# Kernel optimization log

Measured on AMD Instinct MI355X. Metric: run time of the kernel, lower is better.

The kernel has to match this reference:

```python
import jax, jax.numpy as jnp
import numpy as np

B, Q, K, D, H = 16, 128, 128, 512, 512
NEG = -1e6


def setup_inputs() -> dict:
    key = jax.random.key(0)
    ks = jax.random.split(key, 7)
    return {
        "queries": jax.random.normal(ks[0], (B, Q, D), dtype=jnp.float32),
        "keys": jax.random.normal(ks[1], (B, K, D), dtype=jnp.float32),
        "values": jax.random.normal(ks[2], (B, K, D), dtype=jnp.float32),
        "valid_lens": jax.random.randint(ks[3], (B,), 1, K + 1, dtype=jnp.int32),
        "Wq": jax.random.normal(ks[4], (D, H), dtype=jnp.float32) / np.sqrt(D),
        "Wk": jax.random.normal(ks[5], (D, H), dtype=jnp.float32) / np.sqrt(D),
        "wv": jax.random.normal(ks[6], (H,), dtype=jnp.float32) / np.sqrt(H),
    }


def reference(queries, keys, values, valid_lens, Wq, Wk, wv):
    # projections (LazyLinear, bias=False)
    q = jnp.einsum("bqd,dh->bqh", queries, Wq)  # [B,Q,H]
    k = jnp.einsum("bkd,dh->bkh", keys, Wk)    # [B,K,H]
    # broadcast add -> tanh -> reduce to scalar score (Bahdanau)
    feats = jnp.tanh(q[:, :, None, :] + k[:, None, :, :])  # [B,Q,K,H]
    scores = jnp.einsum("bqkh,h->bqk", feats, wv)           # [B,Q,K]
    # masked softmax over key dim using per-batch valid lengths
    mask = jnp.arange(scores.shape[-1])[None, None, :] < valid_lens[:, None, None]
    scores = jnp.where(mask, scores, NEG)
    attn = jax.nn.softmax(scores, axis=-1)                  # [B,Q,K]
    # dropout is identity in eval mode
    return jnp.einsum("bqk,bkv->bqv", attn, values)
```

## Files before the change

### kernel.cpp

```cpp
#include <hip/hip_runtime.h>

#define Bn 16
#define Qn 128
#define Kn 128
#define Dn 512
#define Hn 512
#define NEGV (-3.0e38f)
#define PSCALE 2.8853900817779268f

typedef short s16x8 __attribute__((ext_vector_type(8)));
typedef float f32x4 __attribute__((ext_vector_type(4)));

__device__ __forceinline__ float exp2_hw(float x) {
  float r;
  asm("v_exp_f32 %0, %1" : "=v"(r) : "v"(x));
  return r;
}
__device__ __forceinline__ float rcp_hw(float x) { return __builtin_amdgcn_rcpf(x); }
__device__ __forceinline__ unsigned short f2bf(float f) {
  unsigned int u = __float_as_uint(f);
  u += 0x7fff + ((u >> 16) & 1);
  return (unsigned short)(u >> 16);
}

__global__ __launch_bounds__(256) void convert_kernel(
    const float* __restrict__ queries, const float* __restrict__ keys,
    const float* __restrict__ Wq, const float* __restrict__ Wk,
    const float* __restrict__ values,
    unsigned short* __restrict__ Abf, unsigned short* __restrict__ Wt,
    unsigned short* __restrict__ Vt)
{
  const int bid = blockIdx.x, t = threadIdx.x;
  if (bid < 512) {
    const int gid = bid * 256 + t;
    const size_t base = (size_t)gid * 16;
    const float* src = (base < 1048576) ? (queries + base) : (keys + (base - 1048576));
    unsigned short o[16];
    #pragma unroll
    for (int j = 0; j < 4; ++j) {
      float4 v = *(const float4*)(src + j * 4);
      o[j * 4 + 0] = f2bf(v.x); o[j * 4 + 1] = f2bf(v.y);
      o[j * 4 + 2] = f2bf(v.z); o[j * 4 + 3] = f2bf(v.w);
    }
    #pragma unroll
    for (int j = 0; j < 4; ++j)
      *(ushort4*)(Abf + base + j * 4) = *(ushort4*)&o[j * 4];
  } else if (bid < 640) {
    const int tid = (bid - 512) * 256 + t;
    const int n = tid & 511, rest = tid >> 9;
    const int sel = rest >> 5, k16 = rest & 31;
    const float* W = sel ? Wk : Wq;
    unsigned short o[16];
    #pragma unroll
    for (int i = 0; i < 16; ++i)
      o[i] = f2bf(W[(size_t)(k16 * 16 + i) * Hn + n]);
    unsigned short* dst = Wt + (size_t)sel * 262144 + (size_t)n * 512 + k16 * 16;
    #pragma unroll
    for (int j = 0; j < 4; ++j) *(ushort4*)(dst + j * 4) = *(ushort4*)&o[j * 4];
  } else {
    const int tid = (bid - 640) * 256 + t;
    const int d = tid & 511, rest = tid >> 9;
    const int b = rest >> 2, k32 = rest & 3;
    unsigned short o[32];
    #pragma unroll
    for (int i = 0; i < 32; ++i)
      o[i] = f2bf(values[((size_t)(b * Kn + k32 * 32 + i)) * Dn + d]);
    unsigned short* dst = Vt + (size_t)b * 65536 + (size_t)d * 128 + k32 * 32;
    #pragma unroll
    for (int j = 0; j < 8; ++j) *(ushort4*)(dst + j * 4) = *(ushort4*)&o[j * 4];
  }
}

__global__ __launch_bounds__(256) void proj_mfma(
    const unsigned short* __restrict__ Abf, const unsigned short* __restrict__ Wt,
    const float* __restrict__ wv,
    float* __restrict__ QW, float* __restrict__ Ekq)
{
  __shared__ unsigned short Al[128][72];
  __shared__ unsigned short Bl[64][72];
  __shared__ float Tep[64][132];
  const int t = threadIdx.x, w = t >> 6, l = t & 63;
  const int wm = w >> 1, wn = w & 1;
  const int rowTile = blockIdx.x;
  const int n0 = blockIdx.y * 64;
  const int R0 = rowTile * 128;
  const bool isQ = rowTile < 16;
  const unsigned short* Wsel = Wt + (isQ ? 0 : 262144);

  f32x4 acc[4][2];
  #pragma unroll
  for (int m = 0; m < 4; ++m)
    #pragma unroll
    for (int n = 0; n < 2; ++n) acc[m][n] = (f32x4)0.f;

  const int lr = l & 15, lk = l >> 4;

  for (int k0 = 0; k0 < Hn; k0 += 64) {
    ushort4 ar[4][2], br[2][2];
    #pragma unroll
    for (int i = 0; i < 4; ++i) {
      int g = t + 256 * i, r = g >> 3, c = g & 7;
      const unsigned short* p = Abf + (size_t)(R0 + r) * Hn + k0 + c * 8;
      ar[i][0] = *(const ushort4*)p; ar[i][1] = *(const ushort4*)(p + 4);
    }
    #pragma unroll
    for (int i = 0; i < 2; ++i) {
      int g = t + 256 * i, r = g >> 3, c = g & 7;
      const unsigned short* p = Wsel + (size_t)(n0 + r) * Hn + k0 + c * 8;
      br[i][0] = *(const ushort4*)p; br[i][1] = *(const ushort4*)(p + 4);
    }
    __syncthreads();
    #pragma unroll
    for (int i = 0; i < 4; ++i) {
      int g = t + 256 * i, r = g >> 3, c = g & 7;
      *(ushort4*)&Al[r][c * 8] = ar[i][0]; *(ushort4*)&Al[r][c * 8 + 4] = ar[i][1];
    }
    #pragma unroll
    for (int i = 0; i < 2; ++i) {
      int g = t + 256 * i, r = g >> 3, c = g & 7;
      *(ushort4*)&Bl[r][c * 8] = br[i][0]; *(ushort4*)&Bl[r][c * 8 + 4] = br[i][1];
    }
    __syncthreads();
    #pragma unroll
    for (int ks = 0; ks < 2; ++ks) {
      s16x8 af[4], bf_[2];
      #pragma unroll
      for (int m = 0; m < 4; ++m)
        af[m] = *(const s16x8*)&Al[wm * 64 + m * 16 + lr][ks * 32 + lk * 8];
      #pragma unroll
      for (int n = 0; n < 2; ++n)
        bf_[n] = *(const s16x8*)&Bl[wn * 32 + n * 16 + lr][ks * 32 + lk * 8];
      #pragma unroll
      for (int m = 0; m < 4; ++m)
        #pragma unroll
        for (int n = 0; n < 2; ++n)
          acc[m][n] = __builtin_amdgcn_mfma_f32_16x16x32_bf16(af[m], bf_[n], acc[m][n], 0, 0, 0);
    }
    __syncthreads();
  }

  if (isQ) {
    #pragma unroll
    for (int m = 0; m < 4; ++m)
      #pragma unroll
      for (int n = 0; n < 2; ++n)
        #pragma unroll
        for (int r = 0; r < 4; ++r) {
          int row = R0 + wm * 64 + m * 16 + lk * 4 + r;
          int col = n0 + wn * 32 + n * 16 + lr;
          float a = acc[m][n][r];
          float F  = exp2_hw(-PSCALE * a);
          float WF = -2.f * wv[col] * F;
          float2 o = {WF, F};
          *(float2*)(QW + ((size_t)row * Hn + col) * 2) = o;
        }
  } else {
    const int bb = rowTile - 16;
    #pragma unroll
    for (int m = 0; m < 4; ++m)
      #pragma unroll
      for (int n = 0; n < 2; ++n)
        #pragma unroll
        for (int r = 0; r < 4; ++r) {
          int row_l = wm * 64 + m * 16 + lk * 4 + r;
          int col_l = wn * 32 + n * 16 + lr;
          Tep[col_l][row_l] = exp2_hw(PSCALE * acc[m][n][r]);
        }
    __syncthreads();
    const int hl = t >> 2, kq = (t & 3) * 32;
    float* dst = Ekq + (size_t)bb * 65536 + (size_t)(n0 + hl) * 128 + kq;
    #pragma unroll
    for (int j = 0; j < 8; ++j)
      *(float4*)(dst + j * 4) = *(const float4*)&Tep[hl][kq + j * 4];
  }
}

struct ScoreSet { float4 e0a, e0b, e1a, e1b, qv; };

__device__ __forceinline__ void load_set(ScoreSet& s, const float* ek,
                                         const float* qwp, int hb) {
  const float* ep = ek + (size_t)(2 * hb) * 128;
  s.e0a = *(const float4*)(ep);
  s.e0b = *(const float4*)(ep + 4);
  s.e1a = *(const float4*)(ep + 128);
  s.e1b = *(const float4*)(ep + 132);
  s.qv  = *(const float4*)(qwp + 4 * hb);
}

__device__ __forceinline__ void compute_set(const ScoreSet& s, float acc[8]) {
  const float WF0 = s.qv.x, F0 = s.qv.y, WF1 = s.qv.z, F1 = s.qv.w;
  float d0, d1, num;
  d0 = F0 + s.e0a.x; d1 = F1 + s.e1a.x;
  num = __builtin_fmaf(WF0, d1, WF1 * d0);
  acc[0] = __builtin_fmaf(num, rcp_hw(d0 * d1), acc[0]);
  d0 = F0 + s.e0a.y; d1 = F1 + s.e1a.y;
  num = __builtin_fmaf(WF0, d1, WF1 * d0);
  acc[1] = __builtin_fmaf(num, rcp_hw(d0 * d1), acc[1]);
  d0 = F0 + s.e0a.z; d1 = F1 + s.e1a.z;
  num = __builtin_fmaf(WF0, d1, WF1 * d0);
  acc[2] = __builtin_fmaf(num, rcp_hw(d0 * d1), acc[2]);
  d0 = F0 + s.e0a.w; d1 = F1 + s.e1a.w;
  num = __builtin_fmaf(WF0, d1, WF1 * d0);
  acc[3] = __builtin_fmaf(num, rcp_hw(d0 * d1), acc[3]);
  d0 = F0 + s.e0b.x; d1 = F1 + s.e1b.x;
  num = __builtin_fmaf(WF0, d1, WF1 * d0);
  acc[4] = __builtin_fmaf(num, rcp_hw(d0 * d1), acc[4]);
  d0 = F0 + s.e0b.y; d1 = F1 + s.e1b.y;
  num = __builtin_fmaf(WF0, d1, WF1 * d0);
  acc[5] = __builtin_fmaf(num, rcp_hw(d0 * d1), acc[5]);
  d0 = F0 + s.e0b.z; d1 = F1 + s.e1b.z;
  num = __builtin_fmaf(WF0, d1, WF1 * d0);
  acc[6] = __builtin_fmaf(num, rcp_hw(d0 * d1), acc[6]);
  d0 = F0 + s.e0b.w; d1 = F1 + s.e1b.w;
  num = __builtin_fmaf(WF0, d1, WF1 * d0);
  acc[7] = __builtin_fmaf(num, rcp_hw(d0 * d1), acc[7]);
}

__global__ __launch_bounds__(256) void score_kernel(
    const float* __restrict__ QW, const float* __restrict__ Ekq,
    float* __restrict__ Sp)
{
  const int id = blockIdx.x;
  const int g = id & 127, qt = id >> 7;
  const int b = g >> 3, hs = g & 7;
  const int t = threadIdx.x, w = t >> 6, l = t & 63;
  const int q  = qt * 16 + w * 4 + (l >> 4);
  const int k0 = (l & 15) * 8;
  const int h0 = hs * 64;

  const float* ek  = Ekq + (size_t)b * 65536 + (size_t)h0 * 128 + k0;
  const float* qwp = QW + ((size_t)(b * Qn + q) * Hn + h0) * 2;

  float acc[8];
  #pragma unroll
  for (int j = 0; j < 8; ++j) acc[j] = 0.f;

  ScoreSet sA, sB;
  load_set(sA, ek, qwp, 0);
  load_set(sB, ek, qwp, 1);
  #pragma unroll 4
  for (int hb = 0; hb < 32; hb += 2) {
    compute_set(sA, acc);
    if (hb + 2 < 32) load_set(sA, ek, qwp, hb + 2);
    compute_set(sB, acc);
    if (hb + 3 < 32) load_set(sB, ek, qwp, hb + 3);
  }

  float4 o0 = {acc[0], acc[1], acc[2], acc[3]};
  float4 o1 = {acc[4], acc[5], acc[6], acc[7]};
  size_t sb = (((size_t)hs * Bn + b) * Qn + q) * Kn + k0;
  *(float4*)(Sp + sb) = o0;
  *(float4*)(Sp + sb + 4) = o1;
}

__global__ __launch_bounds__(512) void softmax_kernel(
    const float* __restrict__ Sp, const int* __restrict__ valid_lens,
    unsigned short* __restrict__ At)
{
  const int t = threadIdx.x;
  const int b = blockIdx.y;
  const int q = blockIdx.x * 16 + (t >> 5);
  const int k0 = (t & 31) * 4;
  const size_t base = ((size_t)b * Qn + q) * Kn + k0;

  float s[4] = {0.f, 0.f, 0.f, 0.f};
  #pragma unroll
  for (int p = 0; p < 8; ++p) {
    float4 sv = *(const float4*)(Sp + base + (size_t)p * 262144);
    s[0] += sv.x; s[1] += sv.y; s[2] += sv.z; s[3] += sv.w;
  }

  const int vlen = valid_lens[b];
  bool ok[4];
  float m = NEGV;
  #pragma unroll
  for (int j = 0; j < 4; ++j) {
    ok[j] = (k0 + j) < vlen;
    if (ok[j]) m = fmaxf(m, s[j]);
  }
  #pragma unroll
  for (int xm = 16; xm >= 1; xm >>= 1) m = fmaxf(m, __shfl_xor(m, xm, 32));
  float e[4], sum = 0.f;
  #pragma unroll
  for (int j = 0; j < 4; ++j) {
    e[j] = ok[j] ? exp2_hw((s[j] - m) * 1.44269504f) : 0.f;
    sum += e[j];
  }
  #pragma unroll
  for (int xm = 16; xm >= 1; xm >>= 1) sum += __shfl_xor(sum, xm, 32);
  float inv = rcp_hw(sum);
  ushort4 o = {f2bf(e[0] * inv), f2bf(e[1] * inv), f2bf(e[2] * inv), f2bf(e[3] * inv)};
  *(ushort4*)(At + base) = o;
}

__global__ __launch_bounds__(256) void av_mfma(
    const unsigned short* __restrict__ At, const unsigned short* __restrict__ Vt,
    float* __restrict__ out)
{
  __shared__ unsigned short AtL[128][72];
  __shared__ unsigned short VL[128][72];
  const int t = threadIdx.x, w = t >> 6, l = t & 63;
  const int wm = w >> 1, wn = w & 1;
  const int dt = blockIdx.x;
  const int b = blockIdx.y;
  const int lr = l & 15, lk = l >> 4;

  f32x4 acc[4][4];
  #pragma unroll
  for (int m = 0; m < 4; ++m)
    #pragma unroll
    for (int n = 0; n < 4; ++n) acc[m][n] = (f32x4)0.f;

  const unsigned short* Atb = At + (size_t)b * Qn * Kn;
  const unsigned short* Vtb = Vt + (size_t)b * 65536 + (size_t)dt * 128 * Kn;

  for (int k0 = 0; k0 < Kn; k0 += 64) {
    ushort4 ar[4][2], vr[4][2];
    #pragma unroll
    for (int i = 0; i < 4; ++i) {
      int g = t + 256 * i, r = g >> 3, c = g & 7;
      const unsigned short* p = Atb + (size_t)r * Kn + k0 + c * 8;
      ar[i][0] = *(const ushort4*)p; ar[i][1] = *(const ushort4*)(p + 4);
      const unsigned short* pv = Vtb + (size_t)r * Kn + k0 + c * 8;
      vr[i][0] = *(const ushort4*)pv; vr[i][1] = *(const ushort4*)(pv + 4);
    }
    __syncthreads();
    #pragma unroll
    for (int i = 0; i < 4; ++i) {
      int g = t + 256 * i, r = g >> 3, c = g & 7;
      *(ushort4*)&AtL[r][c * 8] = ar[i][0]; *(ushort4*)&AtL[r][c * 8 + 4] = ar[i][1];
      *(ushort4*)&VL[r][c * 8] = vr[i][0];  *(ushort4*)&VL[r][c * 8 + 4] = vr[i][1];
    }
    __syncthreads();
    #pragma unroll
    for (int ks = 0; ks < 2; ++ks) {
      s16x8 af[4], bf_[4];
      #pragma unroll
      for (int m = 0; m < 4; ++m)
        af[m] = *(const s16x8*)&AtL[wm * 64 + m * 16 + lr][ks * 32 + lk * 8];
      #pragma unroll
      for (int n = 0; n < 4; ++n)
        bf_[n] = *(const s16x8*)&VL[wn * 64 + n * 16 + lr][ks * 32 + lk * 8];
      #pragma unroll
      for (int m = 0; m < 4; ++m)
        #pragma unroll
        for (int n = 0; n < 4; ++n)
          acc[m][n] = __builtin_amdgcn_mfma_f32_16x16x32_bf16(af[m], bf_[n], acc[m][n], 0, 0, 0);
    }
    __syncthreads();
  }

  #pragma unroll
  for (int m = 0; m < 4; ++m)
    #pragma unroll
    for (int n = 0; n < 4; ++n)
      #pragma unroll
      for (int r = 0; r < 4; ++r) {
        int row = wm * 64 + m * 16 + lk * 4 + r;
        int col = dt * 128 + wn * 64 + n * 16 + lr;
        out[((size_t)(b * Qn) + row) * Dn + col] = acc[m][n][r];
      }
}

extern "C" void kernel_launch(void* const* d_in, const int* in_sizes, int n_in,
                              void* d_out, int out_size, void* d_ws, size_t ws_size,
                              hipStream_t stream) {
  const float* queries    = (const float*)d_in[0];
  const float* keys       = (const float*)d_in[1];
  const float* values     = (const float*)d_in[2];
  const int*   valid_lens = (const int*)d_in[3];
  const float* Wq         = (const float*)d_in[4];
  const float* Wk         = (const float*)d_in[5];
  const float* wv         = (const float*)d_in[6];
  float* out = (float*)d_out;

  unsigned short* Abf = (unsigned short*)d_ws;
  unsigned short* Wt  = Abf + 2097152;
  unsigned short* Vt  = Wt + 524288;
  float*          QW  = (float*)(Vt + 1048576);
  float*          Ekq = QW + 2097152;
  float*          Sp  = Ekq + 1048576;
  unsigned short* At  = (unsigned short*)(Sp + 2097152);

  convert_kernel<<<768, 256, 0, stream>>>(queries, keys, Wq, Wk, values, Abf, Wt, Vt);
  proj_mfma<<<dim3(32, 8), 256, 0, stream>>>(Abf, Wt, wv, QW, Ekq);
  score_kernel<<<1024, 256, 0, stream>>>(QW, Ekq, Sp);
  softmax_kernel<<<dim3(8, 16), 512, 0, stream>>>(Sp, valid_lens, At);
  av_mfma<<<dim3(4, 16), 256, 0, stream>>>(At, Vt, out);
}
```

Baseline: 54.93 us.

## Fuse bf16 conversion of activations and values into GEMM loads; stage score inputs in LDS

```diff
diff --git a/kernel.cpp b/kernel.cpp
--- a/kernel.cpp
+++ b/kernel.cpp
@@ -23,57 +23,26 @@
   return (unsigned short)(u >> 16);
 }
 
-__global__ __launch_bounds__(256) void convert_kernel(
+__global__ __launch_bounds__(256) void convert_w(
+    const float* __restrict__ Wq, const float* __restrict__ Wk,
+    unsigned short* __restrict__ Wt)
+{
+  const int tid = blockIdx.x * 256 + threadIdx.x;
+  const int n = tid & 511, rest = tid >> 9;
+  const int sel = rest >> 5, k16 = rest & 31;
+  const float* W = sel ? Wk : Wq;
+  unsigned short o[16];
+  #pragma unroll
+  for (int i = 0; i < 16; ++i)
+    o[i] = f2bf(W[(size_t)(k16 * 16 + i) * Hn + n]);
+  unsigned short* dst = Wt + (size_t)sel * 262144 + (size_t)n * 512 + k16 * 16;
+  #pragma unroll
+  for (int j = 0; j < 4; ++j) *(ushort4*)(dst + j * 4) = *(ushort4*)&o[j * 4];
+}
+
+__global__ __launch_bounds__(256) void proj_mfma(
     const float* __restrict__ queries, const float* __restrict__ keys,
-    const float* __restrict__ Wq, const float* __restrict__ Wk,
-    const float* __restrict__ values,
-    unsigned short* __restrict__ Abf, unsigned short* __restrict__ Wt,
-    unsigned short* __restrict__ Vt)
-{
-  const int bid = blockIdx.x, t = threadIdx.x;
-  if (bid < 512) {
-    const int gid = bid * 256 + t;
-    const size_t base = (size_t)gid * 16;
-    const float* src = (base < 1048576) ? (queries + base) : (keys + (base - 1048576));
-    unsigned short o[16];
-    #pragma unroll
-    for (int j = 0; j < 4; ++j) {
-      float4 v = *(const float4*)(src + j * 4);
-      o[j * 4 + 0] = f2bf(v.x); o[j * 4 + 1] = f2bf(v.y);
-      o[j * 4 + 2] = f2bf(v.z); o[j * 4 + 3] = f2bf(v.w);
-    }
-    #pragma unroll
-    for (int j = 0; j < 4; ++j)
-      *(ushort4*)(Abf + base + j * 4) = *(ushort4*)&o[j * 4];
-  } else if (bid < 640) {
-    const int tid = (bid - 512) * 256 + t;
-    const int n = tid & 511, rest = tid >> 9;
-    const int sel = rest >> 5, k16 = rest & 31;
-    const float* W = sel ? Wk : Wq;
-    unsigned short o[16];
-    #pragma unroll
-    for (int i = 0; i < 16; ++i)
-      o[i] = f2bf(W[(size_t)(k16 * 16 + i) * Hn + n]);
-    unsigned short* dst = Wt + (size_t)sel * 262144 + (size_t)n * 512 + k16 * 16;
-    #pragma unroll
-    for (int j = 0; j < 4; ++j) *(ushort4*)(dst + j * 4) = *(ushort4*)&o[j * 4];
-  } else {
-    const int tid = (bid - 640) * 256 + t;
-    const int d = tid & 511, rest = tid >> 9;
-    const int b = rest >> 2, k32 = rest & 3;
-    unsigned short o[32];
-    #pragma unroll
-    for (int i = 0; i < 32; ++i)
-      o[i] = f2bf(values[((size_t)(b * Kn + k32 * 32 + i)) * Dn + d]);
-    unsigned short* dst = Vt + (size_t)b * 65536 + (size_t)d * 128 + k32 * 32;
-    #pragma unroll
-    for (int j = 0; j < 8; ++j) *(ushort4*)(dst + j * 4) = *(ushort4*)&o[j * 4];
-  }
-}
-
-__global__ __launch_bounds__(256) void proj_mfma(
-    const unsigned short* __restrict__ Abf, const unsigned short* __restrict__ Wt,
-    const float* __restrict__ wv,
+    const unsigned short* __restrict__ Wt, const float* __restrict__ wv,
     float* __restrict__ QW, float* __restrict__ Ekq)
 {
   __shared__ unsigned short Al[128][72];
@@ -85,6 +54,8 @@
   const int n0 = blockIdx.y * 64;
   const int R0 = rowTile * 128;
   const bool isQ = rowTile < 16;
+  const float* Asrc = isQ ? queries : keys;
+  const int rowBase = isQ ? R0 : (R0 - 2048);
   const unsigned short* Wsel = Wt + (isQ ? 0 : 262144);
 
   f32x4 acc[4][2];
@@ -96,12 +67,12 @@
   const int lr = l & 15, lk = l >> 4;
 
   for (int k0 = 0; k0 < Hn; k0 += 64) {
-    ushort4 ar[4][2], br[2][2];
-    #pragma unroll
-    for (int i = 0; i < 4; ++i) {
-      int g = t + 256 * i, r = g >> 3, c = g & 7;
-      const unsigned short* p = Abf + (size_t)(R0 + r) * Hn + k0 + c * 8;
-      ar[i][0] = *(const ushort4*)p; ar[i][1] = *(const ushort4*)(p + 4);
+    float4 afr[8];
+    ushort4 br[2][2];
+    #pragma unroll
+    for (int i = 0; i < 8; ++i) {
+      int g = t + 256 * i, r = g >> 4, c4 = g & 15;
+      afr[i] = *(const float4*)(Asrc + (size_t)(rowBase + r) * Dn + k0 + c4 * 4);
     }
     #pragma unroll
     for (int i = 0; i < 2; ++i) {
@@ -111,9 +82,10 @@
     }
     __syncthreads();
     #pragma unroll
-    for (int i = 0; i < 4; ++i) {
-      int g = t + 256 * i, r = g >> 3, c = g & 7;
-      *(ushort4*)&Al[r][c * 8] = ar[i][0]; *(ushort4*)&Al[r][c * 8 + 4] = ar[i][1];
+    for (int i = 0; i < 8; ++i) {
+      int g = t + 256 * i, r = g >> 4, c4 = g & 15;
+      ushort4 o = {f2bf(afr[i].x), f2bf(afr[i].y), f2bf(afr[i].z), f2bf(afr[i].w)};
+      *(ushort4*)&Al[r][c4 * 4] = o;
     }
     #pragma unroll
     for (int i = 0; i < 2; ++i) {
@@ -175,82 +147,81 @@
   }
 }
 
-struct ScoreSet { float4 e0a, e0b, e1a, e1b, qv; };
-
-__device__ __forceinline__ void load_set(ScoreSet& s, const float* ek,
-                                         const float* qwp, int hb) {
-  const float* ep = ek + (size_t)(2 * hb) * 128;
-  s.e0a = *(const float4*)(ep);
-  s.e0b = *(const float4*)(ep + 4);
-  s.e1a = *(const float4*)(ep + 128);
-  s.e1b = *(const float4*)(ep + 132);
-  s.qv  = *(const float4*)(qwp + 4 * hb);
-}
-
-__device__ __forceinline__ void compute_set(const ScoreSet& s, float acc[8]) {
-  const float WF0 = s.qv.x, F0 = s.qv.y, WF1 = s.qv.z, F1 = s.qv.w;
-  float d0, d1, num;
-  d0 = F0 + s.e0a.x; d1 = F1 + s.e1a.x;
-  num = __builtin_fmaf(WF0, d1, WF1 * d0);
-  acc[0] = __builtin_fmaf(num, rcp_hw(d0 * d1), acc[0]);
-  d0 = F0 + s.e0a.y; d1 = F1 + s.e1a.y;
-  num = __builtin_fmaf(WF0, d1, WF1 * d0);
-  acc[1] = __builtin_fmaf(num, rcp_hw(d0 * d1), acc[1]);
-  d0 = F0 + s.e0a.z; d1 = F1 + s.e1a.z;
-  num = __builtin_fmaf(WF0, d1, WF1 * d0);
-  acc[2] = __builtin_fmaf(num, rcp_hw(d0 * d1), acc[2]);
-  d0 = F0 + s.e0a.w; d1 = F1 + s.e1a.w;
-  num = __builtin_fmaf(WF0, d1, WF1 * d0);
-  acc[3] = __builtin_fmaf(num, rcp_hw(d0 * d1), acc[3]);
-  d0 = F0 + s.e0b.x; d1 = F1 + s.e1b.x;
-  num = __builtin_fmaf(WF0, d1, WF1 * d0);
-  acc[4] = __builtin_fmaf(num, rcp_hw(d0 * d1), acc[4]);
-  d0 = F0 + s.e0b.y; d1 = F1 + s.e1b.y;
-  num = __builtin_fmaf(WF0, d1, WF1 * d0);
-  acc[5] = __builtin_fmaf(num, rcp_hw(d0 * d1), acc[5]);
-  d0 = F0 + s.e0b.z; d1 = F1 + s.e1b.z;
-  num = __builtin_fmaf(WF0, d1, WF1 * d0);
-  acc[6] = __builtin_fmaf(num, rcp_hw(d0 * d1), acc[6]);
-  d0 = F0 + s.e0b.w; d1 = F1 + s.e1b.w;
-  num = __builtin_fmaf(WF0, d1, WF1 * d0);
-  acc[7] = __builtin_fmaf(num, rcp_hw(d0 * d1), acc[7]);
-}
-
 __global__ __launch_bounds__(256) void score_kernel(
     const float* __restrict__ QW, const float* __restrict__ Ekq,
     float* __restrict__ Sp)
 {
+  __shared__ float EkL[8192];
+  __shared__ float QWL[2048];
   const int id = blockIdx.x;
   const int g = id & 127, qt = id >> 7;
   const int b = g >> 3, hs = g & 7;
   const int t = threadIdx.x, w = t >> 6, l = t & 63;
-  const int q  = qt * 16 + w * 4 + (l >> 4);
-  const int k0 = (l & 15) * 8;
-  const int h0 = hs * 64;
-
-  const float* ek  = Ekq + (size_t)b * 65536 + (size_t)h0 * 128 + k0;
-  const float* qwp = QW + ((size_t)(b * Qn + q) * Hn + h0) * 2;
+  const int q_l = w * 4 + (l >> 4);
+  const int ka = (l & 15) * 4;
+
+  {
+    const float4* esrc = (const float4*)(Ekq + (size_t)b * 65536 + (size_t)hs * 8192);
+    float4* edst = (float4*)EkL;
+    #pragma unroll
+    for (int i = 0; i < 8; ++i) edst[t + 256 * i] = esrc[t + 256 * i];
+    const float4* qsrc = (const float4*)QW;
+    float4* qdst = (float4*)QWL;
+    #pragma unroll
+    for (int i = 0; i < 2; ++i) {
+      int idx = t + 256 * i;
+      int qrow = idx >> 5, rest = idx & 31;
+      qdst[idx] = qsrc[(size_t)(b * Qn + qt * 16 + qrow) * 256 + hs * 32 + rest];
+    }
+  }
+  __syncthreads();
 
   float acc[8];
   #pragma unroll
   for (int j = 0; j < 8; ++j) acc[j] = 0.f;
 
-  ScoreSet sA, sB;
-  load_set(sA, ek, qwp, 0);
-  load_set(sB, ek, qwp, 1);
   #pragma unroll 4
-  for (int hb = 0; hb < 32; hb += 2) {
-    compute_set(sA, acc);
-    if (hb + 2 < 32) load_set(sA, ek, qwp, hb + 2);
-    compute_set(sB, acc);
-    if (hb + 3 < 32) load_set(sB, ek, qwp, hb + 3);
-  }
-
+  for (int hb = 0; hb < 32; ++hb) {
+    const float* ekp = EkL + hb * 256;
+    float4 ea0 = *(const float4*)(ekp + ka);
+    float4 ea1 = *(const float4*)(ekp + 64 + ka);
+    float4 eb0 = *(const float4*)(ekp + 128 + ka);
+    float4 eb1 = *(const float4*)(ekp + 192 + ka);
+    float4 qv  = *(const float4*)(QWL + q_l * 128 + hb * 4);
+    const float WF0 = qv.x, F0 = qv.y, WF1 = qv.z, F1 = qv.w;
+    float d0, d1, num;
+    d0 = F0 + ea0.x; d1 = F1 + eb0.x;
+    num = __builtin_fmaf(WF0, d1, WF1 * d0);
+    acc[0] = __builtin_fmaf(num, rcp_hw(d0 * d1), acc[0]);
+    d0 = F0 + ea0.y; d1 = F1 + eb0.y;
+    num = __builtin_fmaf(WF0, d1, WF1 * d0);
+    acc[1] = __builtin_fmaf(num, rcp_hw(d0 * d1), acc[1]);
+    d0 = F0 + ea0.z; d1 = F1 + eb0.z;
+    num = __builtin_fmaf(WF0, d1, WF1 * d0);
+    acc[2] = __builtin_fmaf(num, rcp_hw(d0 * d1), acc[2]);
+    d0 = F0 + ea0.w; d1 = F1 + eb0.w;
+    num = __builtin_fmaf(WF0, d1, WF1 * d0);
+    acc[3] = __builtin_fmaf(num, rcp_hw(d0 * d1), acc[3]);
+    d0 = F0 + ea1.x; d1 = F1 + eb1.x;
+    num = __builtin_fmaf(WF0, d1, WF1 * d0);
+    acc[4] = __builtin_fmaf(num, rcp_hw(d0 * d1), acc[4]);
+    d0 = F0 + ea1.y; d1 = F1 + eb1.y;
+    num = __builtin_fmaf(WF0, d1, WF1 * d0);
+    acc[5] = __builtin_fmaf(num, rcp_hw(d0 * d1), acc[5]);
+    d0 = F0 + ea1.z; d1 = F1 + eb1.z;
+    num = __builtin_fmaf(WF0, d1, WF1 * d0);
+    acc[6] = __builtin_fmaf(num, rcp_hw(d0 * d1), acc[6]);
+    d0 = F0 + ea1.w; d1 = F1 + eb1.w;
+    num = __builtin_fmaf(WF0, d1, WF1 * d0);
+    acc[7] = __builtin_fmaf(num, rcp_hw(d0 * d1), acc[7]);
+  }
+
+  const int q = qt * 16 + q_l;
   float4 o0 = {acc[0], acc[1], acc[2], acc[3]};
   float4 o1 = {acc[4], acc[5], acc[6], acc[7]};
-  size_t sb = (((size_t)hs * Bn + b) * Qn + q) * Kn + k0;
-  *(float4*)(Sp + sb) = o0;
-  *(float4*)(Sp + sb + 4) = o1;
+  size_t sb = (((size_t)hs * Bn + b) * Qn + q) * Kn;
+  *(float4*)(Sp + sb + ka) = o0;
+  *(float4*)(Sp + sb + 64 + ka) = o1;
 }
 
 __global__ __launch_bounds__(512) void softmax_kernel(
@@ -294,7 +265,7 @@
 }
 
 __global__ __launch_bounds__(256) void av_mfma(
-    const unsigned short* __restrict__ At, const unsigned short* __restrict__ Vt,
+    const unsigned short* __restrict__ At, const float* __restrict__ values,
     float* __restrict__ out)
 {
   __shared__ unsigned short AtL[128][72];
@@ -312,24 +283,34 @@
     for (int n = 0; n < 4; ++n) acc[m][n] = (f32x4)0.f;
 
   const unsigned short* Atb = At + (size_t)b * Qn * Kn;
-  const unsigned short* Vtb = Vt + (size_t)b * 65536 + (size_t)dt * 128 * Kn;
 
   for (int k0 = 0; k0 < Kn; k0 += 64) {
-    ushort4 ar[4][2], vr[4][2];
+    ushort4 ar[4][2];
+    float4 vv[8];
     #pragma unroll
     for (int i = 0; i < 4; ++i) {
       int g = t + 256 * i, r = g >> 3, c = g & 7;
       const unsigned short* p = Atb + (size_t)r * Kn + k0 + c * 8;
       ar[i][0] = *(const ushort4*)p; ar[i][1] = *(const ushort4*)(p + 4);
-      const unsigned short* pv = Vtb + (size_t)r * Kn + k0 + c * 8;
-      vr[i][0] = *(const ushort4*)pv; vr[i][1] = *(const ushort4*)(pv + 4);
+    }
+    #pragma unroll
+    for (int j = 0; j < 8; ++j) {
+      int idx = t + 256 * j, k_l = idx >> 5, d4 = idx & 31;
+      vv[j] = *(const float4*)(values + ((size_t)(b * Kn) + k0 + k_l) * Dn + dt * 128 + d4 * 4);
     }
     __syncthreads();
     #pragma unroll
     for (int i = 0; i < 4; ++i) {
       int g = t + 256 * i, r = g >> 3, c = g & 7;
       *(ushort4*)&AtL[r][c * 8] = ar[i][0]; *(ushort4*)&AtL[r][c * 8 + 4] = ar[i][1];
-      *(ushort4*)&VL[r][c * 8] = vr[i][0];  *(ushort4*)&VL[r][c * 8 + 4] = vr[i][1];
+    }
+    #pragma unroll
+    for (int j = 0; j < 8; ++j) {
+      int idx = t + 256 * j, k_l = idx >> 5, d4 = idx & 31;
+      VL[d4 * 4 + 0][k_l] = f2bf(vv[j].x);
+      VL[d4 * 4 + 1][k_l] = f2bf(vv[j].y);
+      VL[d4 * 4 + 2][k_l] = f2bf(vv[j].z);
+      VL[d4 * 4 + 3][k_l] = f2bf(vv[j].w);
     }
     __syncthreads();
     #pragma unroll
@@ -374,17 +355,15 @@
   const float* wv         = (const float*)d_in[6];
   float* out = (float*)d_out;
 
-  unsigned short* Abf = (unsigned short*)d_ws;
-  unsigned short* Wt  = Abf + 2097152;
-  unsigned short* Vt  = Wt + 524288;
-  float*          QW  = (float*)(Vt + 1048576);
+  unsigned short* Wt  = (unsigned short*)d_ws;
+  float*          QW  = (float*)(Wt + 524288);
   float*          Ekq = QW + 2097152;
   float*          Sp  = Ekq + 1048576;
   unsigned short* At  = (unsigned short*)(Sp + 2097152);
 
-  convert_kernel<<<768, 256, 0, stream>>>(queries, keys, Wq, Wk, values, Abf, Wt, Vt);
-  proj_mfma<<<dim3(32, 8), 256, 0, stream>>>(Abf, Wt, wv, QW, Ekq);
+  convert_w<<<128, 256, 0, stream>>>(Wq, Wk, Wt);
+  proj_mfma<<<dim3(32, 8), 256, 0, stream>>>(queries, keys, Wt, wv, QW, Ekq);
   score_kernel<<<1024, 256, 0, stream>>>(QW, Ekq, Sp);
   softmax_kernel<<<dim3(8, 16), 512, 0, stream>>>(Sp, valid_lens, At);
-  av_mfma<<<dim3(4, 16), 256, 0, stream>>>(At, Vt, out);
-}
+  av_mfma<<<dim3(4, 16), 256, 0, stream>>>(At, values, out);
+}
```

Result: faster. 51.79 us (-5.7%).
